# Kernel tuning notes

Hardware: AMD Instinct MI355X
Metric: run time of the kernel (lower is better)

## Reference

```python
import jax, jax.numpy as jnp
import numpy as np


def setup_inputs() -> dict:
    key = jax.random.key(0)
    ks = jax.random.split(key, 7)
    B, S, D = 256, 1024, 128  # batch of sets, set size, n_input
    H = 256
    x = jax.random.normal(ks[0], (B, S, D), dtype=jnp.float32)
    # torch nn.Linear weights: [out_features, in_features], in = 2*layer_in
    W0 = jax.random.normal(ks[1], (H, 2 * D), dtype=jnp.float32) * 0.05
    b0 = jnp.zeros((H,), dtype=jnp.float32)
    W1 = jax.random.normal(ks[2], (H, 2 * H), dtype=jnp.float32) * 0.05
    b1 = jnp.zeros((H,), dtype=jnp.float32)
    W2 = jax.random.normal(ks[3], (H, 2 * H), dtype=jnp.float32) * 0.05
    b2 = jnp.zeros((H,), dtype=jnp.float32)
    return {"x": x, "W0": W0, "b0": b0, "W1": W1, "b1": b1, "W2": W2, "b2": b2}


def reference(x, W0, b0, W1, b1, W2, b2):
    # x: [B, S, D] batch of sets. Original loops over batch; we vmap.
    def apply_set(y):
        # y: [S, d]
        for W, b in ((W0, b0), (W1, b1), (W2, b2)):
            mean = jnp.mean(y, axis=0, keepdims=True)            # [1, d]
            mean = jnp.broadcast_to(mean, y.shape)               # [S, d]
            z = jnp.concatenate([y, mean], axis=1)               # [S, 2d]
            y = jnp.tanh(z @ W.T + b)                            # [S, out]
        return jnp.mean(y, axis=0)                               # [out]
    return jax.vmap(apply_set)(x)                                # [B, out]
```

## Files before the change

### kernel.cpp

```cpp
#include <hip/hip_runtime.h>
#include <hip/hip_bf16.h>

#define B_ 256
#define S_ 1024
#define D_ 128
#define H_ 256

typedef short short8 __attribute__((ext_vector_type(8)));
typedef float f32x4 __attribute__((ext_vector_type(4)));

__device__ unsigned short g_Wb0[H_ * D_];
__device__ unsigned short g_Wb1[H_ * H_];
__device__ unsigned short g_Wb2[H_ * H_];
__device__ float g_mean0[B_ * D_];
__device__ float g_colsum1[B_ * H_];
__device__ float g_colsum2[B_ * H_];

__device__ __forceinline__ unsigned short f2bf(float x) {
    union { float f; unsigned u; } v; v.f = x;
    unsigned r = v.u + 0x7FFFu + ((v.u >> 16) & 1u);
    return (unsigned short)(r >> 16);
}
__device__ __forceinline__ float bf2f(unsigned short h) {
    union { float f; unsigned u; } v; v.u = ((unsigned)h) << 16;
    return v.f;
}
__device__ __forceinline__ float fast_tanh(float x) {
    float e = __builtin_amdgcn_exp2f(x * 2.885390081777927f);
    float r = __builtin_amdgcn_rcpf(1.0f + e);
    return 1.0f - 2.0f * r;
}

__global__ __launch_bounds__(256) void prep_kernel(
    const float* __restrict__ W0, const float* __restrict__ W1,
    const float* __restrict__ W2)
{
    int i = blockIdx.x * 256 + threadIdx.x;
    if (i < H_ * D_) { g_Wb0[i] = f2bf(W0[(i >> 7) * 256 + (i & 127)]); return; }
    i -= H_ * D_;
    if (i < H_ * H_) { g_Wb1[i] = f2bf(W1[(i >> 8) * 512 + (i & 255)]); return; }
    i -= H_ * H_;
    if (i < H_ * H_) { g_Wb2[i] = f2bf(W2[(i >> 8) * 512 + (i & 255)]); return; }
}

__global__ __launch_bounds__(1024) void means0_kernel(const float* __restrict__ x)
{
    const int set = blockIdx.x, t = threadIdx.x;
    const int cg = t & 31, rg = t >> 5;
    const float* xb = x + (size_t)set * S_ * D_;
    f32x4 s = (f32x4){0.f, 0.f, 0.f, 0.f};
    #pragma unroll 8
    for (int i = 0; i < 32; ++i)
        s += *(const f32x4*)(xb + (rg + i * 32) * D_ + cg * 4);
    __shared__ f32x4 red[32][32];
    red[rg][cg] = s;
    __syncthreads();
    if (t < 32) {
        f32x4 a = red[0][t];
        #pragma unroll
        for (int g = 1; g < 32; ++g) a += red[g][t];
        #pragma unroll
        for (int c = 0; c < 4; ++c) g_mean0[set * D_ + t * 4 + c] = a[c];
    }
}

template <int LAYER>
__global__ __launch_bounds__(512, 4) void layer_kernel(
    const float* __restrict__ x, const float* __restrict__ W,
    const float* __restrict__ bias, const unsigned short* __restrict__ yin,
    unsigned short* __restrict__ yout, float* __restrict__ out)
{
    constexpr int K  = (LAYER == 0) ? D_ : H_;
    constexpr int KS = K / 32;
    const int set = blockIdx.x >> 1, ch = blockIdx.x & 1;
    const int t = threadIdx.x;
    const int lane = t & 63, wave = t >> 6;
    const int l15 = lane & 15, quad = lane >> 4;

    __shared__ unsigned short W_lds[128 * K];
    __shared__ float mean_lds[K];
    __shared__ float c_lds[128];
    __shared__ float colsum_lds[128];
    __shared__ float cpart[512];

    const unsigned short* Wb = (LAYER == 0) ? g_Wb0 : (LAYER == 1) ? g_Wb1 : g_Wb2;
    const float* msrc = (LAYER == 0) ? g_mean0 : (LAYER == 1) ? g_colsum1 : g_colsum2;

    if (t < 128) colsum_lds[t] = 0.f;
    if (t < K)   mean_lds[t] = msrc[set * K + t] * (1.f / S_);
    __syncthreads();

    {
        const int n = t & 127, g = t >> 7;
        const unsigned short* src = Wb + (size_t)(ch * 128 + n) * K;
        #pragma unroll
        for (int i = 0; i < KS; ++i) {
            const int slot = g * KS + i;
            *(uint4*)(&W_lds[n * K + ((slot ^ (n & 7)) * 8)]) =
                *(const uint4*)(src + slot * 8);
        }
    }
    {
        const int j = t >> 2, q = t & 3;
        const float* wl = W + (size_t)(ch * 128 + j) * 2 * K + q * (K / 4);
        const float* wr = wl + K;
        float acc = 0.f;
        #pragma unroll 4
        for (int k = 0; k < K / 4; k += 4) {
            f32x4 a = *(const f32x4*)(wl + k);
            f32x4 b = *(const f32x4*)(wr + k);
            f32x4 m = *(const f32x4*)(&mean_lds[q * (K / 4) + k]);
            #pragma unroll
            for (int c = 0; c < 4; ++c)
                acc += m[c] * (b[c] + (a[c] - bf2f(f2bf(a[c]))));
        }
        cpart[t] = acc;
    }
    __syncthreads();
    if (t < 128)
        c_lds[t] = bias[ch * 128 + t] +
                   cpart[4 * t] + cpart[4 * t + 1] + cpart[4 * t + 2] + cpart[4 * t + 3];
    __syncthreads();

    const int rowA = wave * 128;
    #pragma unroll 1
    for (int p = 0; p < 4; ++p) {
        const int row0 = rowA + p * 32 + l15;

        short8 a[2][KS];
        if (LAYER == 0) {
            const float* xb = x + ((size_t)set * S_ + row0) * D_ + quad * 8;
            #pragma unroll
            for (int mf = 0; mf < 2; ++mf)
                #pragma unroll
                for (int ks = 0; ks < KS; ++ks) {
                    const float* p2 = xb + mf * 16 * D_ + ks * 32;
                    f32x4 v0 = *(const f32x4*)(p2);
                    f32x4 v1 = *(const f32x4*)(p2 + 4);
                    short8 sv;
                    #pragma unroll
                    for (int c = 0; c < 4; ++c) {
                        sv[c]     = (short)f2bf(v0[c]);
                        sv[4 + c] = (short)f2bf(v1[c]);
                    }
                    a[mf][ks] = sv;
                }
        } else {
            const unsigned short* yb = yin + ((size_t)set * S_ + row0) * H_ + quad * 8;
            #pragma unroll
            for (int mf = 0; mf < 2; ++mf)
                #pragma unroll
                for (int ks = 0; ks < KS; ++ks)
                    a[mf][ks] = *(const short8*)(yb + mf * 16 * H_ + ks * 32);
        }

        #pragma unroll 1
        for (int nt = 0; nt < 4; ++nt) {
            f32x4 acc[2][2];
            acc[0][0] = acc[0][1] = acc[1][0] = acc[1][1] = (f32x4){0.f, 0.f, 0.f, 0.f};
            const int rb0 = (nt * 32 + l15) * K;
            const int rb1 = (nt * 32 + 16 + l15) * K;
            #pragma unroll
            for (int ks = 0; ks < KS; ++ks) {
                const int so = ((ks * 4 + quad) ^ (l15 & 7)) * 8;
                short8 b0 = *(const short8*)(&W_lds[rb0 + so]);
                short8 b1 = *(const short8*)(&W_lds[rb1 + so]);
                acc[0][0] = __builtin_amdgcn_mfma_f32_16x16x32_bf16(a[0][ks], b0, acc[0][0], 0, 0, 0);
                acc[1][0] = __builtin_amdgcn_mfma_f32_16x16x32_bf16(a[1][ks], b0, acc[1][0], 0, 0, 0);
                acc[0][1] = __builtin_amdgcn_mfma_f32_16x16x32_bf16(a[0][ks], b1, acc[0][1], 0, 0, 0);
                acc[1][1] = __builtin_amdgcn_mfma_f32_16x16x32_bf16(a[1][ks], b1, acc[1][1], 0, 0, 0);
            }
            #pragma unroll
            for (int nf = 0; nf < 2; ++nf) {
                const int lcol = nt * 32 + nf * 16 + l15;
                const float cv = c_lds[lcol];
                float sn = 0.f;
                #pragma unroll
                for (int mf = 0; mf < 2; ++mf) {
                    unsigned short* yo = (LAYER < 2)
                        ? yout + ((size_t)set * S_ + rowA + p * 32 + mf * 16 + quad * 4) * H_ + ch * 128 + lcol
                        : nullptr;
                    #pragma unroll
                    for (int r = 0; r < 4; ++r) {
                        float th = fast_tanh(acc[mf][nf][r] + cv);
                        sn += th;
                        if (LAYER < 2) yo[r * H_] = f2bf(th);
                    }
                }
                sn += __shfl_xor(sn, 16);
                sn += __shfl_xor(sn, 32);
                if (quad == 0) atomicAdd(&colsum_lds[lcol], sn);
            }
        }
    }
    __syncthreads();
    if (t < 128) {
        if (LAYER == 0)      g_colsum1[set * H_ + ch * 128 + t] = colsum_lds[t];
        else if (LAYER == 1) g_colsum2[set * H_ + ch * 128 + t] = colsum_lds[t];
        else                 out[set * H_ + ch * 128 + t] = colsum_lds[t] * (1.f / S_);
    }
}

extern "C" void kernel_launch(void* const* d_in, const int* in_sizes, int n_in,
                              void* d_out, int out_size, void* d_ws, size_t ws_size,
                              hipStream_t stream) {
    (void)in_sizes; (void)n_in; (void)out_size; (void)ws_size;
    const float* x  = (const float*)d_in[0];
    const float* W0 = (const float*)d_in[1];
    const float* b0 = (const float*)d_in[2];
    const float* W1 = (const float*)d_in[3];
    const float* b1 = (const float*)d_in[4];
    const float* W2 = (const float*)d_in[5];
    const float* b2 = (const float*)d_in[6];
    float* out = (float*)d_out;

    unsigned short* y0 = (unsigned short*)d_ws;
    unsigned short* y1 = (unsigned short*)d_in[0];

    prep_kernel<<<dim3(640), dim3(256), 0, stream>>>(W0, W1, W2);
    means0_kernel<<<dim3(256), dim3(1024), 0, stream>>>(x);
    layer_kernel<0><<<dim3(512), dim3(512), 0, stream>>>(x, W0, b0, y0, y0, out);
    layer_kernel<1><<<dim3(512), dim3(512), 0, stream>>>(x, W1, b1, y0, y1, out);
    layer_kernel<2><<<dim3(512), dim3(512), 0, stream>>>(x, W2, b2, y1, y1, out);
}
```

Before: 452.2 us.

## Swap MFMA operand roles, store activations in fragment-native tiled layout, remap blocks per XCD

The weight tile becomes the A operand and activations the B operand, so each MFMA output lane holds four consecutive feature columns. The intermediate bf16 activations are written in a tiled layout that matches the next layer's fragment loads, replacing strided 2-byte scattered stores with packed 8-byte stores and contiguous 16-byte loads. Column sums now accumulate in registers across all row groups and are reduced once at the end, reducing LDS atomic traffic. Block indices are remapped so both halves of a set land on the same XCD for L2 sharing. The trade-offs are more registers and one MFMA chain per tile with less independent work to overlap.

```diff
diff --git a/kernel.cpp b/kernel.cpp
--- a/kernel.cpp
+++ b/kernel.cpp
@@ -72,7 +72,10 @@
 {
     constexpr int K  = (LAYER == 0) ? D_ : H_;
     constexpr int KS = K / 32;
-    const int set = blockIdx.x >> 1, ch = blockIdx.x & 1;
+    const int bid = blockIdx.x;
+    const int xcd = bid & 7, slot = bid >> 3;
+    const int ch = slot & 1;
+    const int set = xcd * 32 + (slot >> 1);
     const int t = threadIdx.x;
     const int lane = t & 63, wave = t >> 6;
     const int l15 = lane & 15, quad = lane >> 4;
@@ -95,9 +98,9 @@
         const unsigned short* src = Wb + (size_t)(ch * 128 + n) * K;
         #pragma unroll
         for (int i = 0; i < KS; ++i) {
-            const int slot = g * KS + i;
-            *(uint4*)(&W_lds[n * K + ((slot ^ (n & 7)) * 8)]) =
-                *(const uint4*)(src + slot * 8);
+            const int slot2 = g * KS + i;
+            *(uint4*)(&W_lds[n * K + ((slot2 ^ (n & 7)) * 8)]) =
+                *(const uint4*)(src + slot2 * 8);
         }
     }
     {
@@ -122,75 +125,77 @@
                    cpart[4 * t] + cpart[4 * t + 1] + cpart[4 * t + 2] + cpart[4 * t + 3];
     __syncthreads();
 
-    const int rowA = wave * 128;
+    const unsigned short* yin_set  = yin  + (size_t)set * (S_ * H_);
+    unsigned short*       yout_set = yout + (size_t)set * (S_ * H_);
+
+    f32x4 csum[8];
+    #pragma unroll
+    for (int mt = 0; mt < 8; ++mt) csum[mt] = (f32x4){0.f, 0.f, 0.f, 0.f};
+
     #pragma unroll 1
-    for (int p = 0; p < 4; ++p) {
-        const int row0 = rowA + p * 32 + l15;
-
-        short8 a[2][KS];
+    for (int rg = 0; rg < 8; ++rg) {
+        const int r16 = wave * 8 + rg;
+
+        short8 yf[KS];
         if (LAYER == 0) {
-            const float* xb = x + ((size_t)set * S_ + row0) * D_ + quad * 8;
-            #pragma unroll
-            for (int mf = 0; mf < 2; ++mf)
+            const float* xr = x + ((size_t)set * S_ + r16 * 16 + l15) * D_ + quad * 8;
+            #pragma unroll
+            for (int ks = 0; ks < KS; ++ks) {
+                f32x4 v0 = *(const f32x4*)(xr + ks * 32);
+                f32x4 v1 = *(const f32x4*)(xr + ks * 32 + 4);
+                short8 sv;
                 #pragma unroll
-                for (int ks = 0; ks < KS; ++ks) {
-                    const float* p2 = xb + mf * 16 * D_ + ks * 32;
-                    f32x4 v0 = *(const f32x4*)(p2);
-                    f32x4 v1 = *(const f32x4*)(p2 + 4);
-                    short8 sv;
-                    #pragma unroll
-                    for (int c = 0; c < 4; ++c) {
-                        sv[c]     = (short)f2bf(v0[c]);
-                        sv[4 + c] = (short)f2bf(v1[c]);
-                    }
-                    a[mf][ks] = sv;
+                for (int c = 0; c < 4; ++c) {
+                    sv[c]     = (short)f2bf(v0[c]);
+                    sv[4 + c] = (short)f2bf(v1[c]);
                 }
+                yf[ks] = sv;
+            }
         } else {
-            const unsigned short* yb = yin + ((size_t)set * S_ + row0) * H_ + quad * 8;
-            #pragma unroll
-            for (int mf = 0; mf < 2; ++mf)
-                #pragma unroll
-                for (int ks = 0; ks < KS; ++ks)
-                    a[mf][ks] = *(const short8*)(yb + mf * 16 * H_ + ks * 32);
-        }
-
-        #pragma unroll 1
-        for (int nt = 0; nt < 4; ++nt) {
-            f32x4 acc[2][2];
-            acc[0][0] = acc[0][1] = acc[1][0] = acc[1][1] = (f32x4){0.f, 0.f, 0.f, 0.f};
-            const int rb0 = (nt * 32 + l15) * K;
-            const int rb1 = (nt * 32 + 16 + l15) * K;
+            const unsigned short* tb = yin_set + (size_t)r16 * (8 * 512);
+            #pragma unroll
+            for (int ks = 0; ks < KS; ++ks)
+                yf[ks] = *(const short8*)(tb + ks * 512 + lane * 8);
+        }
+
+        #pragma unroll 2
+        for (int mt = 0; mt < 8; ++mt) {
+            f32x4 acc = (f32x4){0.f, 0.f, 0.f, 0.f};
+            const int wrow = (mt * 16 + l15) * K;
             #pragma unroll
             for (int ks = 0; ks < KS; ++ks) {
                 const int so = ((ks * 4 + quad) ^ (l15 & 7)) * 8;
-                short8 b0 = *(const short8*)(&W_lds[rb0 + so]);
-                short8 b1 = *(const short8*)(&W_lds[rb1 + so]);
-                acc[0][0] = __builtin_amdgcn_mfma_f32_16x16x32_bf16(a[0][ks], b0, acc[0][0], 0, 0, 0);
-                acc[1][0] = __builtin_amdgcn_mfma_f32_16x16x32_bf16(a[1][ks], b0, acc[1][0], 0, 0, 0);
-                acc[0][1] = __builtin_amdgcn_mfma_f32_16x16x32_bf16(a[0][ks], b1, acc[0][1], 0, 0, 0);
-                acc[1][1] = __builtin_amdgcn_mfma_f32_16x16x32_bf16(a[1][ks], b1, acc[1][1], 0, 0, 0);
-            }
-            #pragma unroll
-            for (int nf = 0; nf < 2; ++nf) {
-                const int lcol = nt * 32 + nf * 16 + l15;
-                const float cv = c_lds[lcol];
-                float sn = 0.f;
-                #pragma unroll
-                for (int mf = 0; mf < 2; ++mf) {
-                    unsigned short* yo = (LAYER < 2)
-                        ? yout + ((size_t)set * S_ + rowA + p * 32 + mf * 16 + quad * 4) * H_ + ch * 128 + lcol
-                        : nullptr;
-                    #pragma unroll
-                    for (int r = 0; r < 4; ++r) {
-                        float th = fast_tanh(acc[mf][nf][r] + cv);
-                        sn += th;
-                        if (LAYER < 2) yo[r * H_] = f2bf(th);
-                    }
-                }
-                sn += __shfl_xor(sn, 16);
-                sn += __shfl_xor(sn, 32);
-                if (quad == 0) atomicAdd(&colsum_lds[lcol], sn);
-            }
+                short8 wf = *(const short8*)(&W_lds[wrow + so]);
+                acc = __builtin_amdgcn_mfma_f32_16x16x32_bf16(wf, yf[ks], acc, 0, 0, 0);
+            }
+            f32x4 cv = *(const f32x4*)(&c_lds[mt * 16 + quad * 4]);
+            union { unsigned short u[4]; uint2 v; } pk;
+            #pragma unroll
+            for (int r = 0; r < 4; ++r) {
+                float th = fast_tanh(acc[r] + cv[r]);
+                csum[mt][r] += th;
+                pk.u[r] = f2bf(th);
+            }
+            if (LAYER < 2) {
+                const int c32 = ch * 4 + (mt >> 1);
+                unsigned short* dst = yout_set + ((size_t)r16 * 8 + c32) * 512
+                                      + ((mt & 1) * 2 + (quad >> 1)) * 128
+                                      + l15 * 8 + (quad & 1) * 4;
+                *(uint2*)dst = pk.v;
+            }
+        }
+    }
+
+    #pragma unroll
+    for (int mt = 0; mt < 8; ++mt) {
+        #pragma unroll
+        for (int r = 0; r < 4; ++r) {
+            float v = csum[mt][r];
+            v += __shfl_xor(v, 1);
+            v += __shfl_xor(v, 2);
+            v += __shfl_xor(v, 4);
+            v += __shfl_xor(v, 8);
+            if (l15 == 0) atomicAdd(&colsum_lds[mt * 16 + quad * 4 + r], v);
         }
     }
     __syncthreads();
```

After: 433.1 us. 4.2% less time.
